# Kernel optimization log

Measured on AMD Instinct MI355X. Metric: run time of the kernel, lower is better.

The kernel has to match this reference:

```python
import jax, jax.numpy as jnp
import numpy as np

B, T = 1024, 200
IN_DIM, COND_DIM, H, OUT_DIM = 3, 4, 128, 3
TF_RATIO = 0.5


def setup_inputs() -> dict:
    key = jax.random.key(0)
    ks = jax.random.split(key, 16)
    s_c = 1.0 / np.sqrt(COND_DIM)
    s_h = 1.0 / np.sqrt(H)
    inp = {
        "conds": jax.random.normal(ks[0], (B, COND_DIM), jnp.float32),
        "target_seq": jax.random.normal(ks[1], (B, T, IN_DIM), jnp.float32),
        "lengths": jax.random.randint(ks[2], (B,), 0, T, jnp.int32),
        "tf_rand": jax.random.uniform(ks[3], (T, B), jnp.float32),
        # fc_cond
        "Wc": jax.random.uniform(ks[4], (COND_DIM, H), jnp.float32, -s_c, s_c),
        "bc": jax.random.uniform(ks[5], (H,), jnp.float32, -s_c, s_c),
        # LSTM layer 0 (input = IN_DIM + H); gate order i,f,g,o as in torch
        "W_ih0": jax.random.uniform(ks[6], (IN_DIM + H, 4 * H), jnp.float32, -s_h, s_h),
        "W_hh0": jax.random.uniform(ks[7], (H, 4 * H), jnp.float32, -s_h, s_h),
        "b0": jax.random.uniform(ks[8], (4 * H,), jnp.float32, -s_h, s_h),
        # LSTM layer 1 (input = H)
        "W_ih1": jax.random.uniform(ks[9], (H, 4 * H), jnp.float32, -s_h, s_h),
        "W_hh1": jax.random.uniform(ks[10], (H, 4 * H), jnp.float32, -s_h, s_h),
        "b1": jax.random.uniform(ks[11], (4 * H,), jnp.float32, -s_h, s_h),
        # fc_out
        "Wo": jax.random.uniform(ks[12], (H, OUT_DIM), jnp.float32, -s_h, s_h),
        "bo": jax.random.uniform(ks[13], (OUT_DIM,), jnp.float32, -s_h, s_h),
    }
    return inp


def _lstm_cell(x, h, c, W_ih, W_hh, b):
    z = x @ W_ih + h @ W_hh + b          # [B, 4H]
    i, f, g, o = jnp.split(z, 4, axis=-1)
    c = jax.nn.sigmoid(f) * c + jax.nn.sigmoid(i) * jnp.tanh(g)
    h = jax.nn.sigmoid(o) * jnp.tanh(c)
    return h, c


def reference(conds, target_seq, lengths, tf_rand, Wc, bc,
              W_ih0, W_hh0, b0, W_ih1, W_hh1, b1, Wo, bo):
    cond_embed = conds @ Wc + bc                      # [B, H]
    h0 = jnp.zeros((conds.shape[0], H), conds.dtype)
    carry0 = (h0, h0, h0, h0, jnp.zeros((conds.shape[0], OUT_DIM), conds.dtype))

    def step(carry, xs):
        h0, c0, h1, c1, prev = carry
        tgt_t, rand_t, t = xs                          # [B,3], [B], scalar
        x = jnp.concatenate([prev, cond_embed], axis=-1)  # [B, 3+H]
        h0, c0 = _lstm_cell(x, h0, c0, W_ih0, W_hh0, b0)
        h1, c1 = _lstm_cell(h0, h1, c1, W_ih1, W_hh1, b1)
        pred = h1 @ Wo + bo                            # [B, 3]
        use_tf = (rand_t < TF_RATIO) & (t < lengths)   # per-sample teacher forcing
        prev = jnp.where(use_tf[:, None], tgt_t, pred)
        return (h0, c0, h1, c1, prev), pred

    xs = (jnp.swapaxes(target_seq, 0, 1), tf_rand, jnp.arange(tf_rand.shape[0]))
    _, preds = jax.lax.scan(step, carry0, xs)          # [T, B, 3]
    return jnp.swapaxes(preds, 0, 1)                   # [B, T, 3]
```

## Files before the change

### kernel.cpp

```cpp
#include <hip/hip_runtime.h>


#define BB 1024
#define TT 200
#define INDIM 3
#define CDIM 4
#define HH 128
#define OD 3
#define GG 512
#define EPB 16
#define LDA 264
#define W1F_OFF 65536
#define WF_TOTAL 196608

#define A1_OFF    8448
#define WLDS_OFF  16896
#define B1T_OFF   57856
#define WOT_OFF   59904
#define PREVS_OFF 61440
#define SMEM_SZ   61696

typedef _Float16 f16x8 __attribute__((ext_vector_type(8)));
typedef _Float16 f16x4 __attribute__((ext_vector_type(4)));
typedef float f32x4 __attribute__((ext_vector_type(4)));

__device__ __forceinline__ float sigf(float x) {
    return __fdividef(1.f, 1.f + __expf(-x));
}
__device__ __forceinline__ float tanhfast(float x) {
    return 1.f - __fdividef(2.f, __expf(2.f * x) + 1.f);
}
__device__ __forceinline__ void pinA(uint4& v) {
    asm volatile("" : "+a"(v.x), "+a"(v.y), "+a"(v.z), "+a"(v.w));
}

__global__ void repack_frag_kernel(const float* __restrict__ Whh0,
                                   const float* __restrict__ Wih1,
                                   const float* __restrict__ Whh1,
                                   _Float16* __restrict__ wf) {
    int idx = blockIdx.x * 256 + threadIdx.x;
    if (idx < 65536) {
        int nt = idx >> 11;
        int ks = (idx >> 9) & 3;
        int l  = (idx >> 3) & 63;
        int j  = idx & 7;
        int k  = ks * 32 + ((l >> 4) << 3) + j;
        int col = nt * 16 + (l & 15);
        wf[idx] = (_Float16)Whh0[k * GG + col];
    } else {
        int i2 = idx - 65536;
        int nt = i2 >> 12;
        int ks = (i2 >> 9) & 7;
        int l  = (i2 >> 3) & 63;
        int j  = i2 & 7;
        int k  = ks * 32 + ((l >> 4) << 3) + j;
        int col = nt * 16 + (l & 15);
        float v = (k < HH) ? Wih1[k * GG + col] : Whh1[(k - HH) * GG + col];
        wf[idx] = (_Float16)v;
    }
}

__global__ __attribute__((amdgpu_waves_per_eu(2, 2)))
__launch_bounds__(512) void dubins_lstm_mfma_kernel(
    const float* __restrict__ conds,
    const float* __restrict__ target_seq,
    const int*   __restrict__ lengths,
    const float* __restrict__ tf_rand,
    const float* __restrict__ Wc,
    const float* __restrict__ bc,
    const float* __restrict__ Wih0,
    const float* __restrict__ b0,
    const float* __restrict__ b1,
    const float* __restrict__ Wo,
    const float* __restrict__ bo,
    const _Float16* __restrict__ wf,
    float* __restrict__ out)
{
    __shared__ __align__(16) unsigned char smem[SMEM_SZ];
    _Float16* A0    = (_Float16*)smem;
    _Float16* A1    = (_Float16*)(smem + A1_OFF);
    uint4*    wldsU = (uint4*)(smem + WLDS_OFF);
    float*    cembL = (float*)(smem + WLDS_OFF);
    float*    b1t   = (float*)(smem + B1T_OFF);
    float*    WoT   = (float*)(smem + WOT_OFF);
    float*    prevs = (float*)(smem + PREVS_OFF);

    const int tid  = threadIdx.x;
    const int w    = tid >> 6;
    const int l    = tid & 63;
    const int lo16 = l & 15;
    const int lhi  = l >> 4;
    const int b_base = blockIdx.x * EPB;
    const int om = tid >> 5;
    const int pl = tid & 31;

    for (int i = tid; i < 4224; i += 512) ((unsigned int*)smem)[i] = 0u;
    if (tid < 64) prevs[tid] = 0.f;
    {
        int fw = tid >> 6, fq = (tid >> 4) & 3, fu = tid & 15;
        b1t[tid] = b1[(fw + 8 * fq) * 16 + fu];
    }
    if (tid < 384) WoT[(tid % 3) * 128 + tid / 3] = Wo[tid];

    {
        int m  = tid >> 5;
        int k0 = (tid & 31) * 4;
        float cd[CDIM];
        #pragma unroll
        for (int d = 0; d < CDIM; ++d) cd[d] = conds[(b_base + m) * CDIM + d];
        #pragma unroll
        for (int kk = 0; kk < 4; ++kk) {
            int k = k0 + kk;
            float v = bc[k];
            #pragma unroll
            for (int d = 0; d < CDIM; ++d) v = fmaf(cd[d], Wc[d * HH + k], v);
            cembL[m * HH + k] = v;
        }
    }
    __syncthreads();

    f16x4 czp[4];
    {
        f32x4 cz[4];
        int colq[4];
        #pragma unroll
        for (int q = 0; q < 4; ++q) {
            colq[q] = (w + 8 * q) * 16 + lo16;
            float bz = b0[colq[q]];
            cz[q] = {bz, bz, bz, bz};
        }
        for (int k = 0; k < HH; ++k) {
            float cv0 = cembL[(lhi * 4 + 0) * HH + k];
            float cv1 = cembL[(lhi * 4 + 1) * HH + k];
            float cv2 = cembL[(lhi * 4 + 2) * HH + k];
            float cv3 = cembL[(lhi * 4 + 3) * HH + k];
            #pragma unroll
            for (int q = 0; q < 4; ++q) {
                float wv = Wih0[(INDIM + k) * GG + colq[q]];
                cz[q][0] = fmaf(cv0, wv, cz[q][0]);
                cz[q][1] = fmaf(cv1, wv, cz[q][1]);
                cz[q][2] = fmaf(cv2, wv, cz[q][2]);
                cz[q][3] = fmaf(cv3, wv, cz[q][3]);
            }
        }
        #pragma unroll
        for (int q = 0; q < 4; ++q)
            #pragma unroll
            for (int r = 0; r < 4; ++r) czp[q][r] = (_Float16)cz[q][r];
        __syncthreads();
    }

    float wprev[4][3];
    #pragma unroll
    for (int q = 0; q < 4; ++q)
        #pragma unroll
        for (int d = 0; d < 3; ++d) wprev[q][d] = Wih0[d * GG + (w + 8 * q) * 16 + lo16];
    const float bov  = (pl < OD) ? bo[pl] : 0.f;
    const int   plen = lengths[b_base + om];

    const uint4* __restrict__ w0g = reinterpret_cast<const uint4*>(wf) + (w * 256 + l);
    const uint4* __restrict__ w1g = reinterpret_cast<const uint4*>(wf + W1F_OFF) + (w * 512 + l);
    uint4 w0r[16];
    uint4 w1r[27];
    #pragma unroll
    for (int f = 0; f < 16; ++f) {
        int ks = f >> 2, q = f & 3;
        w0r[f] = w0g[q * 2048 + ks * 64];
        pinA(w0r[f]);
    }
    #pragma unroll
    for (int f = 0; f < 27; ++f) {
        int ks = f >> 2, q = f & 3;
        w1r[f] = w1g[q * 4096 + ks * 64];
        pinA(w1r[f]);
    }
    #pragma unroll
    for (int fi = 0; fi < 5; ++fi) {
        int f = 27 + fi, ks = f >> 2, q = f & 3;
        wldsU[(w * 5 + fi) * 64 + l] = w1g[q * 4096 + ks * 64];
    }
    __syncthreads();

    float c0s[4] = {0.f, 0.f, 0.f, 0.f};
    float c1s[4] = {0.f, 0.f, 0.f, 0.f};

    for (int t = 0; t < TT; ++t) {
        _Float16* Ac = (t & 1) ? A1 : A0;
        _Float16* An = (t & 1) ? A0 : A1;
        const f16x8* apC = reinterpret_cast<const f16x8*>(Ac + lo16 * LDA);
        const f16x8* apN = reinterpret_cast<const f16x8*>(An + lo16 * LDA);

        const float tfv = tf_rand[t * BB + b_base + om];
        float tgtv = 0.f;
        if (pl < OD) tgtv = target_seq[((b_base + om) * TT + t) * OD + pl];

        f32x4 acc[4];

        #pragma unroll
        for (int q = 0; q < 4; ++q)
            acc[q] = {(float)czp[q][0], (float)czp[q][1],
                      (float)czp[q][2], (float)czp[q][3]};
        #pragma unroll
        for (int r = 0; r < 4; ++r) {
            const float4 pv = *reinterpret_cast<const float4*>(prevs + (lhi * 4 + r) * 4);
            #pragma unroll
            for (int q = 0; q < 4; ++q)
                acc[q][r] = fmaf(pv.z, wprev[q][2],
                            fmaf(pv.y, wprev[q][1],
                            fmaf(pv.x, wprev[q][0], acc[q][r])));
        }
        #pragma unroll
        for (int ks = 0; ks < 4; ++ks) {
            const f16x8 a = apC[ks * 4 + lhi];
            #pragma unroll
            for (int q = 0; q < 4; ++q)
                acc[q] = __builtin_amdgcn_mfma_f32_16x16x32_f16(
                             a, __builtin_bit_cast(f16x8, w0r[ks * 4 + q]), acc[q], 0, 0, 0);
        }

        #pragma unroll
        for (int r = 0; r < 4; ++r) {
            const float zi = acc[0][r], zf = acc[1][r], zg = acc[2][r], zo = acc[3][r];
            c0s[r] = sigf(zf) * c0s[r] + sigf(zi) * tanhfast(zg);
            An[(lhi * 4 + r) * LDA + w * 16 + lo16] = (_Float16)(sigf(zo) * tanhfast(c0s[r]));
        }
        __syncthreads();

        #pragma unroll
        for (int q = 0; q < 4; ++q) {
            const float bv = b1t[(w * 4 + q) * 16 + lo16];
            acc[q] = {bv, bv, bv, bv};
        }
        #pragma unroll
        for (int ks = 0; ks < 8; ++ks) {
            const f16x8 a = (ks < 4) ? apN[ks * 4 + lhi]
                                     : apC[16 + (ks - 4) * 4 + lhi];
            #pragma unroll
            for (int q = 0; q < 4; ++q) {
                const int f = ks * 4 + q;
                f16x8 b;
                if (f < 27) b = __builtin_bit_cast(f16x8, w1r[f]);
                else        b = __builtin_bit_cast(f16x8, wldsU[(w * 5 + (f - 27)) * 64 + l]);
                acc[q] = __builtin_amdgcn_mfma_f32_16x16x32_f16(a, b, acc[q], 0, 0, 0);
            }
        }

        #pragma unroll
        for (int r = 0; r < 4; ++r) {
            const float zi = acc[0][r], zf = acc[1][r], zg = acc[2][r], zo = acc[3][r];
            c1s[r] = sigf(zf) * c1s[r] + sigf(zi) * tanhfast(zg);
            An[(lhi * 4 + r) * LDA + HH + w * 16 + lo16] = (_Float16)(sigf(zo) * tanhfast(c1s[r]));
        }
        __syncthreads();

        {
            const f16x4 hv = *reinterpret_cast<const f16x4*>(An + om * LDA + HH + pl * 4);
            const float h0_ = (float)hv[0], h1_ = (float)hv[1],
                        h2_ = (float)hv[2], h3_ = (float)hv[3];
            const float4 wv0 = *reinterpret_cast<const float4*>(WoT + 0 * 128 + pl * 4);
            const float4 wv1 = *reinterpret_cast<const float4*>(WoT + 1 * 128 + pl * 4);
            const float4 wv2 = *reinterpret_cast<const float4*>(WoT + 2 * 128 + pl * 4);
            float s0 = fmaf(h3_, wv0.w, fmaf(h2_, wv0.z, fmaf(h1_, wv0.y, h0_ * wv0.x)));
            float s1 = fmaf(h3_, wv1.w, fmaf(h2_, wv1.z, fmaf(h1_, wv1.y, h0_ * wv1.x)));
            float s2 = fmaf(h3_, wv2.w, fmaf(h2_, wv2.z, fmaf(h1_, wv2.y, h0_ * wv2.x)));
            #pragma unroll
            for (int sh = 16; sh >= 1; sh >>= 1) {
                s0 += __shfl_xor(s0, sh, 32);
                s1 += __shfl_xor(s1, sh, 32);
                s2 += __shfl_xor(s2, sh, 32);
            }
            if (pl < OD) {
                const float sv = (pl == 0) ? s0 : (pl == 1) ? s1 : s2;
                const float pred = sv + bov;
                const int bg = b_base + om;
                out[(bg * TT + t) * OD + pl] = pred;
                const bool use_tf = (tfv < 0.5f) && (t < plen);
                prevs[om * 4 + pl] = use_tf ? tgtv : pred;
            }
        }
        __syncthreads();
    }
}

extern "C" void kernel_launch(void* const* d_in, const int* in_sizes, int n_in,
                              void* d_out, int out_size, void* d_ws, size_t ws_size,
                              hipStream_t stream) {
    const float* conds   = (const float*)d_in[0];
    const float* target  = (const float*)d_in[1];
    const int*   lengths = (const int*)d_in[2];
    const float* tfr     = (const float*)d_in[3];
    const float* Wc      = (const float*)d_in[4];
    const float* bc      = (const float*)d_in[5];
    const float* Wih0    = (const float*)d_in[6];
    const float* Whh0    = (const float*)d_in[7];
    const float* b0      = (const float*)d_in[8];
    const float* Wih1    = (const float*)d_in[9];
    const float* Whh1    = (const float*)d_in[10];
    const float* b1      = (const float*)d_in[11];
    const float* Wo      = (const float*)d_in[12];
    const float* bo      = (const float*)d_in[13];
    float* out = (float*)d_out;
    _Float16* wf = (_Float16*)d_ws;

    repack_frag_kernel<<<WF_TOTAL / 256, 256, 0, stream>>>(Whh0, Wih1, Whh1, wf);
    dubins_lstm_mfma_kernel<<<BB / EPB, 512, 0, stream>>>(
        conds, target, lengths, tfr, Wc, bc,
        Wih0, b0, b1, Wo, bo, wf, out);
}
```

Baseline: 1.426 ms.

## Stream half of layer-1 weights from global each step instead of registers/LDS

Cuts the register-resident layer-1 weight fragments from 27 to 16 and removes the LDS copy of the rest. The other 16 fragments (the W_hh1 half) are reloaded from global memory/L2 every timestep in two batches, issued early so they overlap the layer-0 work. The per-thread constant gate bias is moved from registers into LDS as fp16. This frees registers and LDS, possibly for higher occupancy or less spilling, at the cost of about 256 bytes of global load per thread per step on the serial critical path.

After: 1.317 ms. 7.7% less time.

```diff
diff --git a/kernel.cpp b/kernel.cpp
--- a/kernel.cpp
+++ b/kernel.cpp
@@ -14,11 +14,11 @@
 #define WF_TOTAL 196608
 
 #define A1_OFF    8448
-#define WLDS_OFF  16896
-#define B1T_OFF   57856
-#define WOT_OFF   59904
-#define PREVS_OFF 61440
-#define SMEM_SZ   61696
+#define CZL_OFF   16896
+#define B1T_OFF   33280
+#define WOT_OFF   35328
+#define PREVS_OFF 36864
+#define SMEM_SZ   37120
 
 typedef _Float16 f16x8 __attribute__((ext_vector_type(8)));
 typedef _Float16 f16x4 __attribute__((ext_vector_type(4)));
@@ -79,8 +79,8 @@
     __shared__ __align__(16) unsigned char smem[SMEM_SZ];
     _Float16* A0    = (_Float16*)smem;
     _Float16* A1    = (_Float16*)(smem + A1_OFF);
-    uint4*    wldsU = (uint4*)(smem + WLDS_OFF);
-    float*    cembL = (float*)(smem + WLDS_OFF);
+    _Float16* czLh  = (_Float16*)(smem + CZL_OFF);
+    float*    cembL = (float*)(smem + CZL_OFF);
     float*    b1t   = (float*)(smem + B1T_OFF);
     float*    WoT   = (float*)(smem + WOT_OFF);
     float*    prevs = (float*)(smem + PREVS_OFF);
@@ -119,7 +119,6 @@
     }
     __syncthreads();
 
-    f16x4 czp[4];
     {
         f32x4 cz[4];
         int colq[4];
@@ -143,11 +142,12 @@
                 cz[q][3] = fmaf(cv3, wv, cz[q][3]);
             }
         }
+        __syncthreads();
         #pragma unroll
         for (int q = 0; q < 4; ++q)
             #pragma unroll
-            for (int r = 0; r < 4; ++r) czp[q][r] = (_Float16)cz[q][r];
-        __syncthreads();
+            for (int r = 0; r < 4; ++r)
+                czLh[(q >> 1) * 4096 + tid * 8 + (q & 1) * 4 + r] = (_Float16)cz[q][r];
     }
 
     float wprev[4][3];
@@ -161,23 +161,16 @@
     const uint4* __restrict__ w0g = reinterpret_cast<const uint4*>(wf) + (w * 256 + l);
     const uint4* __restrict__ w1g = reinterpret_cast<const uint4*>(wf + W1F_OFF) + (w * 512 + l);
     uint4 w0r[16];
-    uint4 w1r[27];
+    uint4 w1r[16];
     #pragma unroll
     for (int f = 0; f < 16; ++f) {
-        int ks = f >> 2, q = f & 3;
-        w0r[f] = w0g[q * 2048 + ks * 64];
+        w0r[f] = w0g[(f & 3) * 2048 + (f >> 2) * 64];
         pinA(w0r[f]);
     }
     #pragma unroll
-    for (int f = 0; f < 27; ++f) {
-        int ks = f >> 2, q = f & 3;
-        w1r[f] = w1g[q * 4096 + ks * 64];
+    for (int f = 0; f < 16; ++f) {
+        w1r[f] = w1g[(f & 3) * 4096 + (f >> 2) * 64];
         pinA(w1r[f]);
-    }
-    #pragma unroll
-    for (int fi = 0; fi < 5; ++fi) {
-        int f = 27 + fi, ks = f >> 2, q = f & 3;
-        wldsU[(w * 5 + fi) * 64 + l] = w1g[q * 4096 + ks * 64];
     }
     __syncthreads();
 
@@ -190,16 +183,32 @@
         const f16x8* apC = reinterpret_cast<const f16x8*>(Ac + lo16 * LDA);
         const f16x8* apN = reinterpret_cast<const f16x8*>(An + lo16 * LDA);
 
+        unsigned zofs = 0;
+        asm volatile("" : "+v"(zofs));
+        const uint4* w1s = reinterpret_cast<const uint4*>(
+            reinterpret_cast<const unsigned char*>(w1g) + zofs);
+
+        uint4 sA[8];
+        #pragma unroll
+        for (int fi = 0; fi < 8; ++fi) {
+            const int ks = 4 + (fi >> 2), q = fi & 3;
+            sA[fi] = w1s[q * 4096 + ks * 64];
+        }
+
         const float tfv = tf_rand[t * BB + b_base + om];
         float tgtv = 0.f;
         if (pl < OD) tgtv = target_seq[((b_base + om) * TT + t) * OD + pl];
 
         f32x4 acc[4];
 
-        #pragma unroll
-        for (int q = 0; q < 4; ++q)
-            acc[q] = {(float)czp[q][0], (float)czp[q][1],
-                      (float)czp[q][2], (float)czp[q][3]};
+        {
+            const f16x8 cz01 = *reinterpret_cast<const f16x8*>(czLh + tid * 8);
+            const f16x8 cz23 = *reinterpret_cast<const f16x8*>(czLh + 4096 + tid * 8);
+            acc[0] = {(float)cz01[0], (float)cz01[1], (float)cz01[2], (float)cz01[3]};
+            acc[1] = {(float)cz01[4], (float)cz01[5], (float)cz01[6], (float)cz01[7]};
+            acc[2] = {(float)cz23[0], (float)cz23[1], (float)cz23[2], (float)cz23[3]};
+            acc[3] = {(float)cz23[4], (float)cz23[5], (float)cz23[6], (float)cz23[7]};
+        }
         #pragma unroll
         for (int r = 0; r < 4; ++r) {
             const float4 pv = *reinterpret_cast<const float4*>(prevs + (lhi * 4 + r) * 4);
@@ -224,6 +233,13 @@
             c0s[r] = sigf(zf) * c0s[r] + sigf(zi) * tanhfast(zg);
             An[(lhi * 4 + r) * LDA + w * 16 + lo16] = (_Float16)(sigf(zo) * tanhfast(c0s[r]));
         }
+
+        uint4 sB[8];
+        #pragma unroll
+        for (int fi = 0; fi < 8; ++fi) {
+            const int ks = 6 + (fi >> 2), q = fi & 3;
+            sB[fi] = w1s[q * 4096 + ks * 64];
+        }
         __syncthreads();
 
         #pragma unroll
@@ -237,10 +253,10 @@
                                      : apC[16 + (ks - 4) * 4 + lhi];
             #pragma unroll
             for (int q = 0; q < 4; ++q) {
-                const int f = ks * 4 + q;
                 f16x8 b;
-                if (f < 27) b = __builtin_bit_cast(f16x8, w1r[f]);
-                else        b = __builtin_bit_cast(f16x8, wldsU[(w * 5 + (f - 27)) * 64 + l]);
+                if (ks < 4)      b = __builtin_bit_cast(f16x8, w1r[ks * 4 + q]);
+                else if (ks < 6) b = __builtin_bit_cast(f16x8, sA[(ks - 4) * 4 + q]);
+                else             b = __builtin_bit_cast(f16x8, sB[(ks - 6) * 4 + q]);
                 acc[q] = __builtin_amdgcn_mfma_f32_16x16x32_f16(a, b, acc[q], 0, 0, 0);
             }
         }
```

## Halve block size to 4 waves, each owning two gate column groups in registers

Applied to the files above, without the earlier changes.

The LSTM kernel now runs 256 threads (4 waves) per block instead of 512. Each wave handles two 16-column groups per gate, so all layer-0 weights sit in VGPRs and all layer-1 weights in AGPRs, and the LDS-resident spill of layer-1 weight fragments is gone. The cond-embedding gate bias and b1 move into LDS and are reloaded every step, and the output projection reduction is reshaped for 16 lanes per sample. The intent is fewer waves to synchronise per barrier and no per-step LDS weight reads. The cost is twice the MFMA and activation work per wave on the serial critical path and higher register pressure at one wave per EU.

New measurement: 1.578 ms. 10.6% more time.

```diff
diff --git a/kernel.cpp b/kernel.cpp
--- a/kernel.cpp
+++ b/kernel.cpp
@@ -9,16 +9,17 @@
 #define OD 3
 #define GG 512
 #define EPB 16
+#define TPB 256
 #define LDA 264
 #define W1F_OFF 65536
 #define WF_TOTAL 196608
 
 #define A1_OFF    8448
-#define WLDS_OFF  16896
-#define B1T_OFF   57856
-#define WOT_OFF   59904
-#define PREVS_OFF 61440
-#define SMEM_SZ   61696
+#define CZL_OFF   16896
+#define B1L_OFF   33280
+#define WOT_OFF   41472
+#define PREVS_OFF 43008
+#define SMEM_SZ   43264
 
 typedef _Float16 f16x8 __attribute__((ext_vector_type(8)));
 typedef _Float16 f16x4 __attribute__((ext_vector_type(4)));
@@ -29,6 +30,9 @@
 }
 __device__ __forceinline__ float tanhfast(float x) {
     return 1.f - __fdividef(2.f, __expf(2.f * x) + 1.f);
+}
+__device__ __forceinline__ void pinV(uint4& v) {
+    asm volatile("" : "+v"(v.x), "+v"(v.y), "+v"(v.z), "+v"(v.w));
 }
 __device__ __forceinline__ void pinA(uint4& v) {
     asm volatile("" : "+a"(v.x), "+a"(v.y), "+a"(v.z), "+a"(v.w));
@@ -60,8 +64,8 @@
     }
 }
 
-__global__ __attribute__((amdgpu_waves_per_eu(2, 2)))
-__launch_bounds__(512) void dubins_lstm_mfma_kernel(
+__global__ __attribute__((amdgpu_waves_per_eu(1, 1)))
+__launch_bounds__(TPB) void dubins_lstm_mfma_kernel(
     const float* __restrict__ conds,
     const float* __restrict__ target_seq,
     const int*   __restrict__ lengths,
@@ -79,9 +83,9 @@
     __shared__ __align__(16) unsigned char smem[SMEM_SZ];
     _Float16* A0    = (_Float16*)smem;
     _Float16* A1    = (_Float16*)(smem + A1_OFF);
-    uint4*    wldsU = (uint4*)(smem + WLDS_OFF);
-    float*    cembL = (float*)(smem + WLDS_OFF);
-    float*    b1t   = (float*)(smem + B1T_OFF);
+    _Float16* czL   = (_Float16*)(smem + CZL_OFF);
+    float*    cembL = (float*)(smem + CZL_OFF);
+    float*    b1L   = (float*)(smem + B1L_OFF);
     float*    WoT   = (float*)(smem + WOT_OFF);
     float*    prevs = (float*)(smem + PREVS_OFF);
 
@@ -91,25 +95,21 @@
     const int lo16 = l & 15;
     const int lhi  = l >> 4;
     const int b_base = blockIdx.x * EPB;
-    const int om = tid >> 5;
-    const int pl = tid & 31;
-
-    for (int i = tid; i < 4224; i += 512) ((unsigned int*)smem)[i] = 0u;
+    const int om = tid >> 4;
+    const int pl = tid & 15;
+
+    for (int i = tid; i < 4224; i += TPB) ((unsigned int*)smem)[i] = 0u;
     if (tid < 64) prevs[tid] = 0.f;
+    for (int i = tid; i < 384; i += TPB) WoT[(i % 3) * 128 + i / 3] = Wo[i];
+
     {
-        int fw = tid >> 6, fq = (tid >> 4) & 3, fu = tid & 15;
-        b1t[tid] = b1[(fw + 8 * fq) * 16 + fu];
-    }
-    if (tid < 384) WoT[(tid % 3) * 128 + tid / 3] = Wo[tid];
-
-    {
-        int m  = tid >> 5;
-        int k0 = (tid & 31) * 4;
+        int m  = tid >> 4;
+        int k0 = (tid & 15) * 8;
         float cd[CDIM];
         #pragma unroll
         for (int d = 0; d < CDIM; ++d) cd[d] = conds[(b_base + m) * CDIM + d];
         #pragma unroll
-        for (int kk = 0; kk < 4; ++kk) {
+        for (int kk = 0; kk < 8; ++kk) {
             int k = k0 + kk;
             float v = bc[k];
             #pragma unroll
@@ -119,70 +119,95 @@
     }
     __syncthreads();
 
-    f16x4 czp[4];
+    int colgx[2][4];
+    #pragma unroll
+    for (int g = 0; g < 2; ++g)
+        #pragma unroll
+        for (int x = 0; x < 4; ++x)
+            colgx[g][x] = x * 128 + (w + 4 * g) * 16 + lo16;
+
     {
-        f32x4 cz[4];
-        int colq[4];
-        #pragma unroll
-        for (int q = 0; q < 4; ++q) {
-            colq[q] = (w + 8 * q) * 16 + lo16;
-            float bz = b0[colq[q]];
-            cz[q] = {bz, bz, bz, bz};
-        }
+        f32x4 cz[2][4];
+        #pragma unroll
+        for (int g = 0; g < 2; ++g)
+            #pragma unroll
+            for (int x = 0; x < 4; ++x) {
+                float bz = b0[colgx[g][x]];
+                cz[g][x] = {bz, bz, bz, bz};
+            }
         for (int k = 0; k < HH; ++k) {
             float cv0 = cembL[(lhi * 4 + 0) * HH + k];
             float cv1 = cembL[(lhi * 4 + 1) * HH + k];
             float cv2 = cembL[(lhi * 4 + 2) * HH + k];
             float cv3 = cembL[(lhi * 4 + 3) * HH + k];
             #pragma unroll
-            for (int q = 0; q < 4; ++q) {
-                float wv = Wih0[(INDIM + k) * GG + colq[q]];
-                cz[q][0] = fmaf(cv0, wv, cz[q][0]);
-                cz[q][1] = fmaf(cv1, wv, cz[q][1]);
-                cz[q][2] = fmaf(cv2, wv, cz[q][2]);
-                cz[q][3] = fmaf(cv3, wv, cz[q][3]);
-            }
-        }
-        #pragma unroll
-        for (int q = 0; q < 4; ++q)
-            #pragma unroll
-            for (int r = 0; r < 4; ++r) czp[q][r] = (_Float16)cz[q][r];
+            for (int g = 0; g < 2; ++g)
+                #pragma unroll
+                for (int x = 0; x < 4; ++x) {
+                    float wv = Wih0[(INDIM + k) * GG + colgx[g][x]];
+                    cz[g][x][0] = fmaf(cv0, wv, cz[g][x][0]);
+                    cz[g][x][1] = fmaf(cv1, wv, cz[g][x][1]);
+                    cz[g][x][2] = fmaf(cv2, wv, cz[g][x][2]);
+                    cz[g][x][3] = fmaf(cv3, wv, cz[g][x][3]);
+                }
+        }
         __syncthreads();
+        #pragma unroll
+        for (int g = 0; g < 2; ++g)
+            #pragma unroll
+            for (int h = 0; h < 2; ++h) {
+                f16x8 p;
+                #pragma unroll
+                for (int xi = 0; xi < 2; ++xi)
+                    #pragma unroll
+                    for (int r = 0; r < 4; ++r)
+                        p[xi * 4 + r] = (_Float16)cz[g][h * 2 + xi][r];
+                *reinterpret_cast<f16x8*>(czL + (g * 2 + h) * 2048 + tid * 8) = p;
+            }
+        #pragma unroll
+        for (int g = 0; g < 2; ++g) {
+            float4 bv;
+            bv.x = b1[colgx[g][0]]; bv.y = b1[colgx[g][1]];
+            bv.z = b1[colgx[g][2]]; bv.w = b1[colgx[g][3]];
+            *reinterpret_cast<float4*>(b1L + g * 1024 + tid * 4) = bv;
+        }
     }
 
-    float wprev[4][3];
+    float wp[2][4][3];
     #pragma unroll
-    for (int q = 0; q < 4; ++q)
-        #pragma unroll
-        for (int d = 0; d < 3; ++d) wprev[q][d] = Wih0[d * GG + (w + 8 * q) * 16 + lo16];
+    for (int g = 0; g < 2; ++g)
+        #pragma unroll
+        for (int x = 0; x < 4; ++x)
+            #pragma unroll
+            for (int d = 0; d < 3; ++d)
+                wp[g][x][d] = Wih0[d * GG + colgx[g][x]];
     const float bov  = (pl < OD) ? bo[pl] : 0.f;
     const int   plen = lengths[b_base + om];
 
-    const uint4* __restrict__ w0g = reinterpret_cast<const uint4*>(wf) + (w * 256 + l);
-    const uint4* __restrict__ w1g = reinterpret_cast<const uint4*>(wf + W1F_OFF) + (w * 512 + l);
-    uint4 w0r[16];
-    uint4 w1r[27];
+    const uint4* __restrict__ wf4  = reinterpret_cast<const uint4*>(wf);
+    const uint4* __restrict__ w1f4 = reinterpret_cast<const uint4*>(wf + W1F_OFF);
+    uint4 w0r[2][4][4];
+    uint4 w1r[2][4][8];
     #pragma unroll
-    for (int f = 0; f < 16; ++f) {
-        int ks = f >> 2, q = f & 3;
-        w0r[f] = w0g[q * 2048 + ks * 64];
-        pinA(w0r[f]);
-    }
-    #pragma unroll
-    for (int f = 0; f < 27; ++f) {
-        int ks = f >> 2, q = f & 3;
-        w1r[f] = w1g[q * 4096 + ks * 64];
-        pinA(w1r[f]);
-    }
-    #pragma unroll
-    for (int fi = 0; fi < 5; ++fi) {
-        int f = 27 + fi, ks = f >> 2, q = f & 3;
-        wldsU[(w * 5 + fi) * 64 + l] = w1g[q * 4096 + ks * 64];
-    }
+    for (int g = 0; g < 2; ++g)
+        #pragma unroll
+        for (int x = 0; x < 4; ++x) {
+            const int nt = x * 8 + w + 4 * g;
+            #pragma unroll
+            for (int ks = 0; ks < 4; ++ks) {
+                w0r[g][x][ks] = wf4[nt * 256 + ks * 64 + l];
+                pinV(w0r[g][x][ks]);
+            }
+            #pragma unroll
+            for (int ks = 0; ks < 8; ++ks) {
+                w1r[g][x][ks] = w1f4[nt * 512 + ks * 64 + l];
+                pinA(w1r[g][x][ks]);
+            }
+        }
     __syncthreads();
 
-    float c0s[4] = {0.f, 0.f, 0.f, 0.f};
-    float c1s[4] = {0.f, 0.f, 0.f, 0.f};
+    float c0s[2][4] = {{0.f,0.f,0.f,0.f},{0.f,0.f,0.f,0.f}};
+    float c1s[2][4] = {{0.f,0.f,0.f,0.f},{0.f,0.f,0.f,0.f}};
 
     for (int t = 0; t < TT; ++t) {
         _Float16* Ac = (t & 1) ? A1 : A0;
@@ -194,80 +219,112 @@
         float tgtv = 0.f;
         if (pl < OD) tgtv = target_seq[((b_base + om) * TT + t) * OD + pl];
 
-        f32x4 acc[4];
-
-        #pragma unroll
-        for (int q = 0; q < 4; ++q)
-            acc[q] = {(float)czp[q][0], (float)czp[q][1],
-                      (float)czp[q][2], (float)czp[q][3]};
+        f32x4 acc[2][4];
+
+        #pragma unroll
+        for (int g = 0; g < 2; ++g)
+            #pragma unroll
+            for (int h = 0; h < 2; ++h) {
+                const f16x8 cv = *reinterpret_cast<const f16x8*>(
+                    czL + (g * 2 + h) * 2048 + tid * 8);
+                acc[g][h*2+0] = {(float)cv[0], (float)cv[1], (float)cv[2], (float)cv[3]};
+                acc[g][h*2+1] = {(float)cv[4], (float)cv[5], (float)cv[6], (float)cv[7]};
+            }
         #pragma unroll
         for (int r = 0; r < 4; ++r) {
             const float4 pv = *reinterpret_cast<const float4*>(prevs + (lhi * 4 + r) * 4);
             #pragma unroll
-            for (int q = 0; q < 4; ++q)
-                acc[q][r] = fmaf(pv.z, wprev[q][2],
-                            fmaf(pv.y, wprev[q][1],
-                            fmaf(pv.x, wprev[q][0], acc[q][r])));
+            for (int g = 0; g < 2; ++g)
+                #pragma unroll
+                for (int x = 0; x < 4; ++x)
+                    acc[g][x][r] = fmaf(pv.z, wp[g][x][2],
+                                   fmaf(pv.y, wp[g][x][1],
+                                   fmaf(pv.x, wp[g][x][0], acc[g][x][r])));
         }
         #pragma unroll
         for (int ks = 0; ks < 4; ++ks) {
             const f16x8 a = apC[ks * 4 + lhi];
             #pragma unroll
-            for (int q = 0; q < 4; ++q)
-                acc[q] = __builtin_amdgcn_mfma_f32_16x16x32_f16(
-                             a, __builtin_bit_cast(f16x8, w0r[ks * 4 + q]), acc[q], 0, 0, 0);
-        }
-
-        #pragma unroll
-        for (int r = 0; r < 4; ++r) {
-            const float zi = acc[0][r], zf = acc[1][r], zg = acc[2][r], zo = acc[3][r];
-            c0s[r] = sigf(zf) * c0s[r] + sigf(zi) * tanhfast(zg);
-            An[(lhi * 4 + r) * LDA + w * 16 + lo16] = (_Float16)(sigf(zo) * tanhfast(c0s[r]));
-        }
+            for (int g = 0; g < 2; ++g)
+                #pragma unroll
+                for (int x = 0; x < 4; ++x)
+                    acc[g][x] = __builtin_amdgcn_mfma_f32_16x16x32_f16(
+                        a, __builtin_bit_cast(f16x8, w0r[g][x][ks]), acc[g][x], 0, 0, 0);
+        }
+
+        #pragma unroll
+        for (int g = 0; g < 2; ++g)
+            #pragma unroll
+            for (int r = 0; r < 4; ++r) {
+                const float zi = acc[g][0][r], zf = acc[g][1][r],
+                            zg = acc[g][2][r], zo = acc[g][3][r];
+                c0s[g][r] = sigf(zf) * c0s[g][r] + sigf(zi) * tanhfast(zg);
+                An[(lhi * 4 + r) * LDA + (w + 4 * g) * 16 + lo16] =
+                    (_Float16)(sigf(zo) * tanhfast(c0s[g][r]));
+            }
         __syncthreads();
 
         #pragma unroll
-        for (int q = 0; q < 4; ++q) {
-            const float bv = b1t[(w * 4 + q) * 16 + lo16];
-            acc[q] = {bv, bv, bv, bv};
+        for (int g = 0; g < 2; ++g) {
+            const float4 bv = *reinterpret_cast<const float4*>(b1L + g * 1024 + tid * 4);
+            acc[g][0] = {bv.x, bv.x, bv.x, bv.x};
+            acc[g][1] = {bv.y, bv.y, bv.y, bv.y};
+            acc[g][2] = {bv.z, bv.z, bv.z, bv.z};
+            acc[g][3] = {bv.w, bv.w, bv.w, bv.w};
         }
         #pragma unroll
         for (int ks = 0; ks < 8; ++ks) {
             const f16x8 a = (ks < 4) ? apN[ks * 4 + lhi]
                                      : apC[16 + (ks - 4) * 4 + lhi];
             #pragma unroll
-            for (int q = 0; q < 4; ++q) {
-                const int f = ks * 4 + q;
-                f16x8 b;
-                if (f < 27) b = __builtin_bit_cast(f16x8, w1r[f]);
-                else        b = __builtin_bit_cast(f16x8, wldsU[(w * 5 + (f - 27)) * 64 + l]);
-                acc[q] = __builtin_amdgcn_mfma_f32_16x16x32_f16(a, b, acc[q], 0, 0, 0);
-            }
-        }
-
-        #pragma unroll
-        for (int r = 0; r < 4; ++r) {
-            const float zi = acc[0][r], zf = acc[1][r], zg = acc[2][r], zo = acc[3][r];
-            c1s[r] = sigf(zf) * c1s[r] + sigf(zi) * tanhfast(zg);
-            An[(lhi * 4 + r) * LDA + HH + w * 16 + lo16] = (_Float16)(sigf(zo) * tanhfast(c1s[r]));
-        }
+            for (int g = 0; g < 2; ++g)
+                #pragma unroll
+                for (int x = 0; x < 4; ++x)
+                    acc[g][x] = __builtin_amdgcn_mfma_f32_16x16x32_f16(
+                        a, __builtin_bit_cast(f16x8, w1r[g][x][ks]), acc[g][x], 0, 0, 0);
+        }
+
+        #pragma unroll
+        for (int g = 0; g < 2; ++g)
+            #pragma unroll
+            for (int r = 0; r < 4; ++r) {
+                const float zi = acc[g][0][r], zf = acc[g][1][r],
+                            zg = acc[g][2][r], zo = acc[g][3][r];
+                c1s[g][r] = sigf(zf) * c1s[g][r] + sigf(zi) * tanhfast(zg);
+                An[(lhi * 4 + r) * LDA + HH + (w + 4 * g) * 16 + lo16] =
+                    (_Float16)(sigf(zo) * tanhfast(c1s[g][r]));
+            }
         __syncthreads();
 
         {
-            const f16x4 hv = *reinterpret_cast<const f16x4*>(An + om * LDA + HH + pl * 4);
-            const float h0_ = (float)hv[0], h1_ = (float)hv[1],
-                        h2_ = (float)hv[2], h3_ = (float)hv[3];
-            const float4 wv0 = *reinterpret_cast<const float4*>(WoT + 0 * 128 + pl * 4);
-            const float4 wv1 = *reinterpret_cast<const float4*>(WoT + 1 * 128 + pl * 4);
-            const float4 wv2 = *reinterpret_cast<const float4*>(WoT + 2 * 128 + pl * 4);
-            float s0 = fmaf(h3_, wv0.w, fmaf(h2_, wv0.z, fmaf(h1_, wv0.y, h0_ * wv0.x)));
-            float s1 = fmaf(h3_, wv1.w, fmaf(h2_, wv1.z, fmaf(h1_, wv1.y, h0_ * wv1.x)));
-            float s2 = fmaf(h3_, wv2.w, fmaf(h2_, wv2.z, fmaf(h1_, wv2.y, h0_ * wv2.x)));
-            #pragma unroll
-            for (int sh = 16; sh >= 1; sh >>= 1) {
-                s0 += __shfl_xor(s0, sh, 32);
-                s1 += __shfl_xor(s1, sh, 32);
-                s2 += __shfl_xor(s2, sh, 32);
+            const f16x8 hv = *reinterpret_cast<const f16x8*>(An + om * LDA + HH + pl * 8);
+            float hf[8];
+            #pragma unroll
+            for (int j = 0; j < 8; ++j) hf[j] = (float)hv[j];
+            float s0, s1, s2;
+            {
+                const float4 wa = *reinterpret_cast<const float4*>(WoT + 0 * 128 + pl * 8);
+                const float4 wb = *reinterpret_cast<const float4*>(WoT + 0 * 128 + pl * 8 + 4);
+                s0 = fmaf(hf[7], wb.w, fmaf(hf[6], wb.z, fmaf(hf[5], wb.y, fmaf(hf[4], wb.x,
+                     fmaf(hf[3], wa.w, fmaf(hf[2], wa.z, fmaf(hf[1], wa.y, hf[0] * wa.x)))))));
+            }
+            {
+                const float4 wa = *reinterpret_cast<const float4*>(WoT + 1 * 128 + pl * 8);
+                const float4 wb = *reinterpret_cast<const float4*>(WoT + 1 * 128 + pl * 8 + 4);
+                s1 = fmaf(hf[7], wb.w, fmaf(hf[6], wb.z, fmaf(hf[5], wb.y, fmaf(hf[4], wb.x,
+                     fmaf(hf[3], wa.w, fmaf(hf[2], wa.z, fmaf(hf[1], wa.y, hf[0] * wa.x)))))));
+            }
+            {
+                const float4 wa = *reinterpret_cast<const float4*>(WoT + 2 * 128 + pl * 8);
+                const float4 wb = *reinterpret_cast<const float4*>(WoT + 2 * 128 + pl * 8 + 4);
+                s2 = fmaf(hf[7], wb.w, fmaf(hf[6], wb.z, fmaf(hf[5], wb.y, fmaf(hf[4], wb.x,
+                     fmaf(hf[3], wa.w, fmaf(hf[2], wa.z, fmaf(hf[1], wa.y, hf[0] * wa.x)))))));
+            }
+            #pragma unroll
+            for (int sh = 8; sh >= 1; sh >>= 1) {
+                s0 += __shfl_xor(s0, sh, 16);
+                s1 += __shfl_xor(s1, sh, 16);
+                s2 += __shfl_xor(s2, sh, 16);
             }
             if (pl < OD) {
                 const float sv = (pl == 0) ? s0 : (pl == 1) ? s1 : s2;
@@ -303,7 +360,7 @@
     _Float16* wf = (_Float16*)d_ws;
 
     repack_frag_kernel<<<WF_TOTAL / 256, 256, 0, stream>>>(Whh0, Wih1, Whh1, wf);
-    dubins_lstm_mfma_kernel<<<BB / EPB, 512, 0, stream>>>(
+    dubins_lstm_mfma_kernel<<<BB / EPB, TPB, 0, stream>>>(
         conds, target, lengths, tfr, Wc, bc,
         Wih0, b0, b1, Wo, bo, wf, out);
 }
```
